# Performance work log

Measured on AMD Instinct MI355X. Metric: run time of the kernel, lower is better.

## Reference

```python
import jax, jax.numpy as jnp
import numpy as np

N = 524288
IN_C = 128
OUT_C = 128
NUM_GRAPHS = 64
NUM_STROKES = 8192
EPS = 1e-5


def setup_inputs() -> dict:
    key = jax.random.key(0)
    ks = jax.random.split(key, 8)
    x = jax.random.normal(ks[0], (N, IN_C), dtype=jnp.float32)
    batch = jnp.sort(jax.random.randint(ks[1], (N,), 0, NUM_GRAPHS))
    stroke_idx = jnp.sort(jax.random.randint(ks[2], (N,), 0, NUM_STROKES))
    s = 1.0 / np.sqrt(IN_C)
    W_max = jax.random.uniform(ks[3], (IN_C, OUT_C), jnp.float32, -s, s)
    b_max = jax.random.uniform(ks[4], (OUT_C,), jnp.float32, -s, s)
    g_max = jnp.ones((OUT_C,), jnp.float32)
    be_max = jnp.zeros((OUT_C,), jnp.float32)
    W_sk = jax.random.uniform(ks[5], (IN_C, OUT_C), jnp.float32, -s, s)
    b_sk = jax.random.uniform(ks[6], (OUT_C,), jnp.float32, -s, s)
    g_sk = jnp.ones((OUT_C,), jnp.float32)
    be_sk = jnp.zeros((OUT_C,), jnp.float32)
    return {"x": x, "batch": batch, "stroke_idx": stroke_idx,
            "W_max": W_max, "b_max": b_max, "g_max": g_max, "be_max": be_max,
            "W_sk": W_sk, "b_sk": b_sk, "g_sk": g_sk, "be_sk": be_sk}


def _mlp(x, W, b, gamma, beta):
    # Linear -> BatchNorm1d (training-mode batch stats, biased var) -> ReLU
    h = x @ W + b
    mu = jnp.mean(h, axis=0)
    var = jnp.mean((h - mu) ** 2, axis=0)
    h = (h - mu) * jax.lax.rsqrt(var + EPS) * gamma + beta
    return jax.nn.relu(h)


def reference(x, batch, stroke_idx, W_max, b_max, g_max, be_max, W_sk, b_sk, g_sk, be_sk):
    pool_max = _mlp(x, W_max, b_max, g_max, be_max)      # (N, F)
    pool_sketch = _mlp(x, W_sk, b_sk, g_sk, be_sk)       # (N, F)
    # segment max-pool per graph / per stroke, then broadcast back to nodes
    gmax = jax.ops.segment_max(pool_max, batch, num_segments=NUM_GRAPHS)       # (G, F)
    smax = jax.ops.segment_max(pool_sketch, stroke_idx, num_segments=NUM_STROKES)  # (S, F)
    pool_max = gmax[batch]          # (N, F)
    pool_sketch = smax[stroke_idx]  # (N, F)
    return jnp.concatenate([pool_sketch, pool_max], axis=1)  # (N, 2F)
```

## Files before the change

kernel.cpp:

```cpp
#include <hip/hip_runtime.h>
#include <hip/hip_bf16.h>
#include <climits>
#include <cstdint>
#include <cfloat>

#define NROWS   524288
#define KDIM    128
#define NGRAPH  64
#define NSTROKE 8192
#define EPSF    1e-5f

typedef __bf16 bf16x8 __attribute__((ext_vector_type(8)));
typedef float  f32x4  __attribute__((ext_vector_type(4)));

#define WT_OFF    0
#define CSUM_OFF  65536
#define CSQ_OFF   66560
#define ST_OFF    67584
#define GT_OFF    (ST_OFF + NSTROKE*KDIM*4)

__device__ __forceinline__ unsigned short f2bf(float f) {
  unsigned int u = __float_as_uint(f);
  u += 0x7fffu + ((u >> 16) & 1u);
  return (unsigned short)(u >> 16);
}
__device__ __forceinline__ int fkey(float f) {
  int b = __float_as_int(f);
  return b >= 0 ? b : (b ^ 0x7fffffff);
}
__device__ __forceinline__ float fdec(int k) {
  int b = k >= 0 ? k : (k ^ 0x7fffffff);
  return __int_as_float(b);
}

__global__ void k_init(const float* __restrict__ Wmax, const float* __restrict__ Wsk,
                       unsigned char* __restrict__ ws) {
  unsigned short* wt = (unsigned short*)(ws + WT_OFF);
  float* csum = (float*)(ws + CSUM_OFF);
  float* csq  = (float*)(ws + CSQ_OFF);
  int* st = (int*)(ws + ST_OFF);
  int* gt = (int*)(ws + GT_OFF);
  int i = blockIdx.x * blockDim.x + threadIdx.x;
  const int total = NSTROKE * KDIM;
  for (; i < total; i += gridDim.x * blockDim.x) {
    st[i] = INT_MIN;
    if (i < NGRAPH * KDIM) gt[i] = INT_MIN;
    if (i < 256) { csum[i] = 0.f; csq[i] = 0.f; }
    if (i < 256 * KDIM) {
      int c = i / KDIM, k = i % KDIM;
      float w = (c < 128) ? Wsk[k * 128 + c] : Wmax[k * 128 + (c - 128)];
      wt[i] = f2bf(w);
    }
  }
}

__global__ __launch_bounds__(256) void k_pass1(const float* __restrict__ x,
                                               const int* __restrict__ batch,
                                               const int* __restrict__ stroke,
                                               unsigned char* __restrict__ ws) {
  __shared__ __align__(16) unsigned short xs[64 * 128];
  const unsigned short* wt = (const unsigned short*)(ws + WT_OFF);
  float* csum = (float*)(ws + CSUM_OFF);
  float* csq  = (float*)(ws + CSQ_OFF);
  int* st = (int*)(ws + ST_OFF);
  int* gt = (int*)(ws + GT_OFF);

  const int tid  = threadIdx.x;
  const int lane = tid & 63;
  const int wv   = tid >> 6;
  const int lr   = lane & 15;
  const int lg   = lane >> 4;

  bf16x8 bfrag[4][4];
#pragma unroll
  for (int ks = 0; ks < 4; ++ks)
#pragma unroll
    for (int n = 0; n < 4; ++n) {
      int c = wv * 64 + n * 16 + lr;
      int k = ks * 32 + lg * 8;
      bfrag[ks][n] = *(const bf16x8*)(wt + c * KDIM + k);
    }

  float sumn[4] = {0.f, 0.f, 0.f, 0.f};
  float sqn[4]  = {0.f, 0.f, 0.f, 0.f};

  const bool isS = (wv < 2);
  const int* __restrict__ segp = isS ? stroke : batch;
  int* __restrict__ tab = isS ? st : gt;
  const int tcol = (isS ? wv : wv - 2) * 64;

  int   curseg = -1;
  float runmax[4] = {-FLT_MAX, -FLT_MAX, -FLT_MAX, -FLT_MAX};

#define FLUSH()                                                               \
  if (curseg >= 0) {                                                          \
    _Pragma("unroll")                                                         \
    for (int n = 0; n < 4; ++n) {                                             \
      float f = runmax[n];                                                    \
      f = fmaxf(f, __shfl_xor(f, 16));                                        \
      f = fmaxf(f, __shfl_xor(f, 32));                                        \
      if (lg == 0) atomicMax(&tab[curseg * KDIM + tcol + n * 16 + lr], fkey(f)); \
    }                                                                         \
  }

  for (int ti = 0; ti < 8; ++ti) {
    const int row0 = (blockIdx.x * 8 + ti) * 64;

#pragma unroll
    for (int it = 0; it < 4; ++it) {
      int e  = it * 2048 + tid * 8;
      int r  = e >> 7;
      int kg = (e & 127) >> 3;
      const float* src = x + (size_t)(row0 + r) * KDIM + kg * 8;
      f32x4 v0 = *(const f32x4*)src;
      f32x4 v1 = *(const f32x4*)(src + 4);
      union { bf16x8 v; unsigned short u[8]; } pk;
      pk.u[0] = f2bf(v0[0]); pk.u[1] = f2bf(v0[1]); pk.u[2] = f2bf(v0[2]); pk.u[3] = f2bf(v0[3]);
      pk.u[4] = f2bf(v1[0]); pk.u[5] = f2bf(v1[1]); pk.u[6] = f2bf(v1[2]); pk.u[7] = f2bf(v1[3]);
      *(bf16x8*)(xs + r * KDIM + ((kg ^ (r & 7)) << 3)) = pk.v;
    }
    int segv = segp[row0 + lane];
    __syncthreads();

    f32x4 acc[4][4];
#pragma unroll
    for (int m = 0; m < 4; ++m)
#pragma unroll
      for (int n = 0; n < 4; ++n) { f32x4 z = {0.f, 0.f, 0.f, 0.f}; acc[m][n] = z; }

#pragma unroll
    for (int ks = 0; ks < 4; ++ks) {
      bf16x8 af[4];
#pragma unroll
      for (int m = 0; m < 4; ++m) {
        int r  = m * 16 + lr;
        int kg = ks * 4 + lg;
        af[m] = *(const bf16x8*)(xs + r * KDIM + ((kg ^ (r & 7)) << 3));
      }
#pragma unroll
      for (int m = 0; m < 4; ++m)
#pragma unroll
        for (int n = 0; n < 4; ++n)
          acc[m][n] = __builtin_amdgcn_mfma_f32_16x16x32_bf16(af[m], bfrag[ks][n], acc[m][n], 0, 0, 0);
    }

    float tm[4];
#pragma unroll
    for (int n = 0; n < 4; ++n) {
      float s = 0.f, q = 0.f, t = -FLT_MAX;
#pragma unroll
      for (int m = 0; m < 4; ++m)
#pragma unroll
        for (int rg = 0; rg < 4; ++rg) {
          float v = acc[m][n][rg];
          s += v; q = fmaf(v, v, q); t = fmaxf(t, v);
        }
      sumn[n] += s; sqn[n] += q; tm[n] = t;
    }

    {
      int pv = __shfl_up(segv, 1);
      unsigned long long mask = __ballot(lane > 0 && pv != segv);
      if (mask == 0ull) {
        int seg0 = __shfl(segv, 0);
        if (seg0 == curseg) {
#pragma unroll
          for (int n = 0; n < 4; ++n) runmax[n] = fmaxf(runmax[n], tm[n]);
        } else {
          FLUSH();
          curseg = seg0;
#pragma unroll
          for (int n = 0; n < 4; ++n) runmax[n] = tm[n];
        }
      } else {
        unsigned long long rem = mask;
        int a = 0;
        while (true) {
          int b = rem ? (int)__builtin_ctzll(rem) : 64;
          int segr = __shfl(segv, a);
          float rm[4] = {-FLT_MAX, -FLT_MAX, -FLT_MAX, -FLT_MAX};
#pragma unroll
          for (int m = 0; m < 4; ++m)
#pragma unroll
            for (int rg = 0; rg < 4; ++rg) {
              int pos = m * 16 + lg * 4 + rg;
              bool in = (pos >= a) && (pos < b);
#pragma unroll
              for (int n = 0; n < 4; ++n)
                rm[n] = in ? fmaxf(rm[n], acc[m][n][rg]) : rm[n];
            }
          if (a == 0 && segr == curseg) {
#pragma unroll
            for (int n = 0; n < 4; ++n) runmax[n] = fmaxf(runmax[n], rm[n]);
          } else {
            FLUSH();
            curseg = segr;
#pragma unroll
            for (int n = 0; n < 4; ++n) runmax[n] = rm[n];
          }
          if (b >= 64) break;
          rem &= rem - 1; a = b;
        }
      }
    }
    __syncthreads();
  }

  FLUSH();

#pragma unroll
  for (int n = 0; n < 4; ++n) {
    sumn[n] += __shfl_xor(sumn[n], 16);
    sumn[n] += __shfl_xor(sumn[n], 32);
    sqn[n]  += __shfl_xor(sqn[n], 16);
    sqn[n]  += __shfl_xor(sqn[n], 32);
  }
  float s = 0.f, q = 0.f;
#pragma unroll
  for (int n = 0; n < 4; ++n) if (n == lg) { s = sumn[n]; q = sqn[n]; }
  atomicAdd(&csum[tid], s);
  atomicAdd(&csq[tid], q);
#undef FLUSH
}

__global__ __launch_bounds__(256) void k_out(const int* __restrict__ batch,
                                             const int* __restrict__ stroke,
                                             const float* __restrict__ g_max,
                                             const float* __restrict__ be_max,
                                             const float* __restrict__ g_sk,
                                             const float* __restrict__ be_sk,
                                             const unsigned char* __restrict__ ws,
                                             float* __restrict__ out) {
  const float* csum = (const float*)(ws + CSUM_OFF);
  const float* csq  = (const float*)(ws + CSQ_OFF);
  const int* st = (const int*)(ws + ST_OFF);
  const int* gt = (const int*)(ws + GT_OFF);

  const int lane = threadIdx.x & 63;
  const int wvid = blockIdx.x * 4 + (threadIdx.x >> 6);
  const int row0 = wvid * 64;
  const bool isS = lane < 32;
  const int  cg  = (isS ? lane : lane - 32) * 4;
  const int* tab  = isS ? st : gt;
  const int* idxp = isS ? stroke : batch;
  const float* gv = isS ? g_sk : g_max;
  const float* bv = isS ? be_sk : be_max;

  const float invN = 1.0f / (float)NROWS;
  f32x4 mu, sc, bb;
#pragma unroll
  for (int j = 0; j < 4; ++j) {
    int cc = (isS ? 0 : 128) + cg + j;
    float m  = csum[cc] * invN;
    float vr = csq[cc] * invN - m * m;
    mu[j] = m;
    sc[j] = gv[cg + j] * rsqrtf(vr + EPSF);
    bb[j] = bv[cg + j];
  }

  f32x4* out4 = (f32x4*)out;
#pragma unroll 4
  for (int r = 0; r < 64; ++r) {
    int row = row0 + r;
    int seg = idxp[row];
    const int4 k4 = *(const int4*)(tab + (size_t)seg * KDIM + cg);
    f32x4 v;
    v[0] = fdec(k4.x); v[1] = fdec(k4.y); v[2] = fdec(k4.z); v[3] = fdec(k4.w);
#pragma unroll
    for (int j = 0; j < 4; ++j) v[j] = fmaxf(0.f, (v[j] - mu[j]) * sc[j] + bb[j]);
    __builtin_nontemporal_store(v, &out4[(size_t)row * 64 + lane]);
  }
}

extern "C" void kernel_launch(void* const* d_in, const int* in_sizes, int n_in,
                              void* d_out, int out_size, void* d_ws, size_t ws_size,
                              hipStream_t stream) {
  const float* x      = (const float*)d_in[0];
  const int*   batch  = (const int*)d_in[1];
  const int*   stroke = (const int*)d_in[2];
  const float* Wmax   = (const float*)d_in[3];
  const float* g_max  = (const float*)d_in[5];
  const float* be_max = (const float*)d_in[6];
  const float* Wsk    = (const float*)d_in[7];
  const float* g_sk   = (const float*)d_in[9];
  const float* be_sk  = (const float*)d_in[10];
  unsigned char* ws = (unsigned char*)d_ws;
  float* out = (float*)d_out;

  k_init <<<2048, 512, 0, stream>>>(Wmax, Wsk, ws);
  k_pass1<<<1024, 256, 0, stream>>>(x, batch, stroke, ws);
  k_out  <<<2048, 256, 0, stream>>>(batch, stroke, g_max, be_max, g_sk, be_sk, ws, out);
}
```

Before: 248.4 us.

## Double-buffer x tiles in pass1 with register prefetch of next tile

Adds a second shared-memory tile and prefetches the next 64-row x tile (and its segment ids) into registers before the MFMA and segment-max work on the current tile. The prefetched values are converted to bf16 and stored into the alternate buffer after compute, which leaves one barrier per iteration. The aim is to hide global-load latency behind compute. In exchange it holds 32 more VGPRs for the prefetch and doubles LDS use, which may lower occupancy.

```diff
diff --git a/kernel.cpp b/kernel.cpp
--- a/kernel.cpp
+++ b/kernel.cpp
@@ -58,7 +58,7 @@
                                                const int* __restrict__ batch,
                                                const int* __restrict__ stroke,
                                                unsigned char* __restrict__ ws) {
-  __shared__ __align__(16) unsigned short xs[64 * 128];
+  __shared__ __align__(16) unsigned short xs[2][64 * 128];
   const unsigned short* wt = (const unsigned short*)(ws + WT_OFF);
   float* csum = (float*)(ws + CSUM_OFF);
   float* csq  = (float*)(ws + CSQ_OFF);
@@ -70,6 +70,8 @@
   const int wv   = tid >> 6;
   const int lr   = lane & 15;
   const int lg   = lane >> 4;
+  const int srow = tid >> 4;
+  const int skg  = tid & 15;
 
   bf16x8 bfrag[4][4];
 #pragma unroll
@@ -103,24 +105,46 @@
     }                                                                         \
   }
 
+#define PF_LOAD(ROW0)                                                         \
+  {                                                                           \
+    _Pragma("unroll")                                                         \
+    for (int it = 0; it < 4; ++it) {                                          \
+      const float* src = x + (size_t)((ROW0) + it * 16 + srow) * KDIM + skg * 8; \
+      pf[it * 2]     = *(const f32x4*)src;                                    \
+      pf[it * 2 + 1] = *(const f32x4*)(src + 4);                              \
+    }                                                                         \
+  }
+
+#define PF_STORE(P)                                                           \
+  {                                                                           \
+    _Pragma("unroll")                                                         \
+    for (int it = 0; it < 4; ++it) {                                          \
+      int r = it * 16 + srow;                                                 \
+      union { bf16x8 v; unsigned short u[8]; } pk;                            \
+      f32x4 v0 = pf[it * 2], v1 = pf[it * 2 + 1];                             \
+      pk.u[0] = f2bf(v0[0]); pk.u[1] = f2bf(v0[1]);                           \
+      pk.u[2] = f2bf(v0[2]); pk.u[3] = f2bf(v0[3]);                           \
+      pk.u[4] = f2bf(v1[0]); pk.u[5] = f2bf(v1[1]);                           \
+      pk.u[6] = f2bf(v1[2]); pk.u[7] = f2bf(v1[3]);                           \
+      *(bf16x8*)(xs[P] + r * KDIM + ((skg ^ (r & 7)) << 3)) = pk.v;           \
+    }                                                                         \
+  }
+
+  const int brow = blockIdx.x * 512;
+  f32x4 pf[8];
+  int segv, segnext;
+
+  PF_LOAD(brow);
+  segv = segp[brow + lane];
+  PF_STORE(0);
+  __syncthreads();
+
+  int cur = 0;
   for (int ti = 0; ti < 8; ++ti) {
-    const int row0 = (blockIdx.x * 8 + ti) * 64;
-
-#pragma unroll
-    for (int it = 0; it < 4; ++it) {
-      int e  = it * 2048 + tid * 8;
-      int r  = e >> 7;
-      int kg = (e & 127) >> 3;
-      const float* src = x + (size_t)(row0 + r) * KDIM + kg * 8;
-      f32x4 v0 = *(const f32x4*)src;
-      f32x4 v1 = *(const f32x4*)(src + 4);
-      union { bf16x8 v; unsigned short u[8]; } pk;
-      pk.u[0] = f2bf(v0[0]); pk.u[1] = f2bf(v0[1]); pk.u[2] = f2bf(v0[2]); pk.u[3] = f2bf(v0[3]);
-      pk.u[4] = f2bf(v1[0]); pk.u[5] = f2bf(v1[1]); pk.u[6] = f2bf(v1[2]); pk.u[7] = f2bf(v1[3]);
-      *(bf16x8*)(xs + r * KDIM + ((kg ^ (r & 7)) << 3)) = pk.v;
-    }
-    int segv = segp[row0 + lane];
-    __syncthreads();
+    if (ti < 7) {
+      PF_LOAD(brow + (ti + 1) * 64);
+      segnext = segp[brow + (ti + 1) * 64 + lane];
+    }
 
     f32x4 acc[4][4];
 #pragma unroll
@@ -135,7 +159,7 @@
       for (int m = 0; m < 4; ++m) {
         int r  = m * 16 + lr;
         int kg = ks * 4 + lg;
-        af[m] = *(const bf16x8*)(xs + r * KDIM + ((kg ^ (r & 7)) << 3));
+        af[m] = *(const bf16x8*)(xs[cur] + r * KDIM + ((kg ^ (r & 7)) << 3));
       }
 #pragma unroll
       for (int m = 0; m < 4; ++m)
@@ -203,7 +227,13 @@
         }
       }
     }
+
+    if (ti < 7) {
+      PF_STORE(cur ^ 1);
+      segv = segnext;
+    }
     __syncthreads();
+    cur ^= 1;
   }
 
   FLUSH();
@@ -221,6 +251,8 @@
   atomicAdd(&csum[tid], s);
   atomicAdd(&csq[tid], q);
 #undef FLUSH
+#undef PF_LOAD
+#undef PF_STORE
 }
 
 __global__ __launch_bounds__(256) void k_out(const int* __restrict__ batch,
```

New measurement: 244.0 us. No clear change (-1.7%).

## Load x directly into MFMA fragments, dropping LDS staging and barriers

Applied to the files above, without the earlier changes.

Each wave now reads its A-fragments of x straight from global memory and converts them to bf16 in registers, so the shared-memory tile, swizzled stores and both __syncthreads are gone. Blocks handle 256 rows instead of 512, and the grid doubles to 2048. The four waves in a block each load the same rows, so global and L2 read traffic for x rises about fourfold. The per-lane access pattern is also less coalesced than the earlier cooperative load.

```diff
diff --git a/kernel.cpp b/kernel.cpp
--- a/kernel.cpp
+++ b/kernel.cpp
@@ -31,6 +31,12 @@
 __device__ __forceinline__ float fdec(int k) {
   int b = k >= 0 ? k : (k ^ 0x7fffffff);
   return __int_as_float(b);
+}
+__device__ __forceinline__ bf16x8 cvt8(f32x4 a, f32x4 b) {
+  bf16x8 r;
+  r[0] = (__bf16)a[0]; r[1] = (__bf16)a[1]; r[2] = (__bf16)a[2]; r[3] = (__bf16)a[3];
+  r[4] = (__bf16)b[0]; r[5] = (__bf16)b[1]; r[6] = (__bf16)b[2]; r[7] = (__bf16)b[3];
+  return r;
 }
 
 __global__ void k_init(const float* __restrict__ Wmax, const float* __restrict__ Wsk,
@@ -58,7 +64,6 @@
                                                const int* __restrict__ batch,
                                                const int* __restrict__ stroke,
                                                unsigned char* __restrict__ ws) {
-  __shared__ __align__(16) unsigned short xs[64 * 128];
   const unsigned short* wt = (const unsigned short*)(ws + WT_OFF);
   float* csum = (float*)(ws + CSUM_OFF);
   float* csq  = (float*)(ws + CSQ_OFF);
@@ -103,24 +108,11 @@
     }                                                                         \
   }
 
-  for (int ti = 0; ti < 8; ++ti) {
-    const int row0 = (blockIdx.x * 8 + ti) * 64;
-
-#pragma unroll
-    for (int it = 0; it < 4; ++it) {
-      int e  = it * 2048 + tid * 8;
-      int r  = e >> 7;
-      int kg = (e & 127) >> 3;
-      const float* src = x + (size_t)(row0 + r) * KDIM + kg * 8;
-      f32x4 v0 = *(const f32x4*)src;
-      f32x4 v1 = *(const f32x4*)(src + 4);
-      union { bf16x8 v; unsigned short u[8]; } pk;
-      pk.u[0] = f2bf(v0[0]); pk.u[1] = f2bf(v0[1]); pk.u[2] = f2bf(v0[2]); pk.u[3] = f2bf(v0[3]);
-      pk.u[4] = f2bf(v1[0]); pk.u[5] = f2bf(v1[1]); pk.u[6] = f2bf(v1[2]); pk.u[7] = f2bf(v1[3]);
-      *(bf16x8*)(xs + r * KDIM + ((kg ^ (r & 7)) << 3)) = pk.v;
-    }
+  const int brow = blockIdx.x * 256;
+
+  for (int ti = 0; ti < 4; ++ti) {
+    const int row0 = brow + ti * 64;
     int segv = segp[row0 + lane];
-    __syncthreads();
 
     f32x4 acc[4][4];
 #pragma unroll
@@ -130,13 +122,16 @@
 
 #pragma unroll
     for (int ks = 0; ks < 4; ++ks) {
+      f32x4 raw0[4], raw1[4];
+#pragma unroll
+      for (int m = 0; m < 4; ++m) {
+        const float* p = x + (size_t)(row0 + m * 16 + lr) * KDIM + ks * 32 + lg * 8;
+        raw0[m] = *(const f32x4*)p;
+        raw1[m] = *(const f32x4*)(p + 4);
+      }
       bf16x8 af[4];
 #pragma unroll
-      for (int m = 0; m < 4; ++m) {
-        int r  = m * 16 + lr;
-        int kg = ks * 4 + lg;
-        af[m] = *(const bf16x8*)(xs + r * KDIM + ((kg ^ (r & 7)) << 3));
-      }
+      for (int m = 0; m < 4; ++m) af[m] = cvt8(raw0[m], raw1[m]);
 #pragma unroll
       for (int m = 0; m < 4; ++m)
 #pragma unroll
@@ -203,7 +198,6 @@
         }
       }
     }
-    __syncthreads();
   }
 
   FLUSH();
@@ -288,6 +282,6 @@
   float* out = (float*)d_out;
 
   k_init <<<2048, 512, 0, stream>>>(Wmax, Wsk, ws);
-  k_pass1<<<1024, 256, 0, stream>>>(x, batch, stroke, ws);
+  k_pass1<<<2048, 256, 0, stream>>>(x, batch, stroke, ws);
   k_out  <<<2048, 256, 0, stream>>>(batch, stroke, g_max, be_max, g_sk, be_sk, ws, out);
 }
```

Result: slower. 284.9 us (+14.7%).
